# Optimization experiments

Hardware: AMD Instinct MI355X
Metric: run time of the kernel (lower is better)

Reference implementation:

```python
import jax, jax.numpy as jnp
import numpy as np

N_NODES = 100000
N_EDGES = 1600000
D_IN, D_HID, N_CLS, N_LAYERS = 128, 256, 10, 3


def setup_inputs() -> dict:
    key = jax.random.key(0)
    ks = jax.random.split(key, 8)
    x = jax.random.normal(ks[0], (N_NODES, D_IN), dtype=jnp.float32)
    edge_index = jax.random.randint(ks[1], (2, N_EDGES), 0, N_NODES, dtype=jnp.int64)
    s = 0.05
    Wl = jax.random.normal(ks[2], (N_LAYERS, D_HID, D_IN), dtype=jnp.float32) * s
    Wr = jax.random.normal(ks[3], (N_LAYERS, D_HID, D_IN), dtype=jnp.float32) * s
    bias = jnp.zeros((N_LAYERS, D_HID), dtype=jnp.float32)
    W1 = jax.random.normal(ks[4], (D_HID, D_HID), dtype=jnp.float32) * s
    b1 = jnp.zeros((D_HID,), dtype=jnp.float32)
    W2 = jax.random.normal(ks[5], (N_CLS, D_HID), dtype=jnp.float32) * s
    b2 = jnp.zeros((N_CLS,), dtype=jnp.float32)
    return {"x": x, "edge_index": edge_index, "Wl": Wl, "Wr": Wr, "bias": bias,
            "W1": W1, "b1": b1, "W2": W2, "b2": b2}


def reference(x, edge_index, Wl, Wr, bias, W1, b1, W2, b2):
    n = x.shape[0]
    src, tgt = edge_index[0], edge_index[1]
    # mean aggregation of source-node features onto targets (SAGEConv aggr='mean')
    deg = jax.ops.segment_sum(jnp.ones(src.shape[0], x.dtype), tgt, num_segments=n)
    agg = jax.ops.segment_sum(x[src], tgt, num_segments=n)  # [N, D_in]
    agg = agg / jnp.clip(deg, 1.0)[:, None]
    # Every layer consumes the ORIGINAL x (per the source forward), so agg is shared.
    h = None
    for l in range(Wl.shape[0]):
        h = jax.nn.relu(agg @ Wl[l].T + x @ Wr[l].T + bias[l])  # [N, D_hid]
    # global_mean_pool over all nodes (single graph)
    pooled = jnp.mean(h, axis=0, keepdims=True)  # [1, D_hid]
    z = jax.nn.relu(pooled @ W1.T + b1)
    z = z @ W2.T + b2
    return jax.nn.log_softmax(z, axis=1)
```

## Files before the change

### kernel.cpp

```cpp
#include <hip/hip_runtime.h>
#include <hip/hip_bf16.h>

#define D_IN  128
#define D_HID 256
#define CBITS 7
#define CSIZE 128
#define EPB   4096
#define CCAP  4096

typedef __bf16 bf16x8 __attribute__((ext_vector_type(8)));
typedef float  f32x4  __attribute__((ext_vector_type(4)));
typedef float  f32x2  __attribute__((ext_vector_type(2)));

__device__ __forceinline__ unsigned short f2bf(float f) {
    unsigned u = __float_as_uint(f);
    u += 0x7FFFu + ((u >> 16) & 1u);
    return (unsigned short)(u >> 16);
}
__device__ __forceinline__ uint2 pack4(float4 v) {
    unsigned lo = (unsigned)f2bf(v.x) | ((unsigned)f2bf(v.y) << 16);
    unsigned hi = (unsigned)f2bf(v.z) | ((unsigned)f2bf(v.w) << 16);
    return make_uint2(lo, hi);
}
__device__ __forceinline__ unsigned packfp8(float4 v) {
    int u = __builtin_amdgcn_cvt_pk_fp8_f32(v.x, v.y, 0, false);
    u = __builtin_amdgcn_cvt_pk_fp8_f32(v.z, v.w, u, true);
    return (unsigned)u;
}
__device__ __forceinline__ void g2lds16(const void* g, void* l) {
    __builtin_amdgcn_global_load_lds(
        (const __attribute__((address_space(1))) unsigned int*)g,
        (__attribute__((address_space(3))) unsigned int*)l, 16, 0, 0);
}
__device__ __forceinline__ void acc16(f32x2* a, uint4 v) {
    a[0] += __builtin_amdgcn_cvt_pk_f32_fp8(v.x, false);
    a[1] += __builtin_amdgcn_cvt_pk_f32_fp8(v.x, true);
    a[2] += __builtin_amdgcn_cvt_pk_f32_fp8(v.y, false);
    a[3] += __builtin_amdgcn_cvt_pk_f32_fp8(v.y, true);
    a[4] += __builtin_amdgcn_cvt_pk_f32_fp8(v.z, false);
    a[5] += __builtin_amdgcn_cvt_pk_f32_fp8(v.z, true);
    a[6] += __builtin_amdgcn_cvt_pk_f32_fp8(v.w, false);
    a[7] += __builtin_amdgcn_cvt_pk_f32_fp8(v.w, true);
}

__global__ __launch_bounds__(256)
void prep(const float* __restrict__ x, unsigned short* __restrict__ xb,
          unsigned char* __restrict__ x8,
          const float* __restrict__ Wr2, const float* __restrict__ Wl2,
          unsigned short* __restrict__ Bsw,
          int* __restrict__ gcur, float* __restrict__ pooled_pad,
          long n16, int NXB, int NCB) {
    const int bid = blockIdx.x;
    const int tid = threadIdx.x;
    if (bid < NXB) {
        const long t = (long)bid * 256 + tid;
        if (t >= n16) return;
        const float4* x4 = (const float4*)x;
        float4 v0 = x4[t * 4], v1 = x4[t * 4 + 1], v2 = x4[t * 4 + 2], v3 = x4[t * 4 + 3];
        uint2 p0 = pack4(v0), p1 = pack4(v1), p2 = pack4(v2), p3 = pack4(v3);
        ((uint4*)xb)[t * 2]     = make_uint4(p0.x, p0.y, p1.x, p1.y);
        ((uint4*)xb)[t * 2 + 1] = make_uint4(p2.x, p2.y, p3.x, p3.y);
        ((uint4*)x8)[t] = make_uint4(packfp8(v0), packfp8(v1), packfp8(v2), packfp8(v3));
    } else if (bid < NXB + 32) {
        const int t_idx = (bid - NXB) * 256 + tid;
        const int lane = t_idx & 63;
        const int rest = t_idx >> 6;
        const int tt   = rest & 3;
        const int wn2  = (rest >> 2) & 3;
        const int kk   = rest >> 4;
        const int j = wn2 * 64 + tt * 16 + (lane & 15);
        const int k = kk * 32 + (lane >> 4) * 8;
        const float* src = (k < 128) ? &Wr2[j * 128 + k] : &Wl2[j * 128 + (k - 128)];
        float4 v0 = *(const float4*)src;
        float4 v1 = *(const float4*)(src + 4);
        uint2 p0 = pack4(v0), p1 = pack4(v1);
        *(uint4*)&Bsw[(long)t_idx * 8] = make_uint4(p0.x, p0.y, p1.x, p1.y);
    } else {
        for (int i = tid; i < NCB * 16; i += 256) gcur[i] = 0;
        for (int i = tid; i < 256 * 16; i += 256) pooled_pad[i] = 0.f;
    }
}

__global__ __launch_bounds__(512)
void coarse_bin(const void* __restrict__ ei, int* __restrict__ gcur,
                unsigned* __restrict__ segc, int E, int NCB) {
    __shared__ unsigned sorted[EPB];
    __shared__ unsigned short bkt[EPB];
    __shared__ int cnt[1024], scn[1024], cur[1024], gbase[1024];
    __shared__ int s_is64;
    const int tid = threadIdx.x;
    const long e0 = (long)blockIdx.x * EPB;
    const int ecnt = (int)min((long)EPB, (long)E - e0);

    if (tid < 64) {
        const int v = ((const int*)ei)[2 * tid + 1];
        const unsigned long long b = __ballot(v != 0);
        if (tid == 0) s_is64 = (b == 0ull);
    }
    for (int i = tid; i < 1024; i += 512) cnt[i] = 0;
    __syncthreads();
    const int is64 = s_is64;

    int sv[8], tv[8];
    #pragma unroll
    for (int k = 0; k < 8; ++k) {
        const int j = tid + k * 512;
        if (j < ecnt) {
            if (is64) {
                sv[k] = (int)((const long long*)ei)[e0 + j];
                tv[k] = (int)((const long long*)ei)[E + e0 + j];
            } else {
                sv[k] = ((const int*)ei)[e0 + j];
                tv[k] = ((const int*)ei)[E + e0 + j];
            }
            atomicAdd(&cnt[tv[k] >> CBITS], 1);
        }
    }
    __syncthreads();

    scn[tid] = cnt[tid];
    scn[tid + 512] = cnt[tid + 512];
    __syncthreads();
    for (int off = 1; off < 1024; off <<= 1) {
        const int v0 = (tid >= off) ? scn[tid - off] : 0;
        const int v1 = (tid + 512 >= off) ? scn[tid + 512 - off] : 0;
        __syncthreads();
        scn[tid] += v0;
        scn[tid + 512] += v1;
        __syncthreads();
    }
    cur[tid] = scn[tid] - cnt[tid];
    cur[tid + 512] = scn[tid + 512] - cnt[tid + 512];
    for (int c = tid; c < NCB; c += 512)
        gbase[c] = cnt[c] ? atomicAdd(&gcur[c * 16], cnt[c]) : 0;
    __syncthreads();

    #pragma unroll
    for (int k = 0; k < 8; ++k) {
        const int j = tid + k * 512;
        if (j < ecnt) {
            const int c = tv[k] >> CBITS;
            const int r = atomicAdd(&cur[c], 1);
            sorted[r] = ((unsigned)sv[k] << CBITS) | (unsigned)(tv[k] & (CSIZE - 1));
            bkt[r] = (unsigned short)c;
        }
    }
    __syncthreads();

    for (int i = tid; i < ecnt; i += 512) {
        const int c = bkt[i];
        const int pos = gbase[c] + (i - (scn[c] - cnt[c]));
        if (pos < CCAP) segc[(long)c * CCAP + pos] = sorted[i];
    }
}

__global__ __launch_bounds__(512)
void refine_gather(const int* __restrict__ gcur, const unsigned* __restrict__ segc,
                   const unsigned char* __restrict__ x8,
                   unsigned short* __restrict__ aggb, int M) {
    __shared__ unsigned order[CCAP];
    __shared__ int degh[CSIZE], scn[CSIZE], cur[CSIZE];
    const int tid = threadIdx.x;
    const int cb = blockIdx.x;
    const int nbase = cb << CBITS;
    const int nn = min(CSIZE, M - nbase);
    const int len = min(gcur[cb * 16], CCAP);
    const unsigned* sp = segc + (long)cb * CCAP;

    if (tid < CSIZE) degh[tid] = 0;
    __syncthreads();
    for (int i = tid; i < len; i += 512) {
        const unsigned e = sp[i];
        atomicAdd(&degh[e & (CSIZE - 1)], 1);
    }
    __syncthreads();
    if (tid < CSIZE) scn[tid] = degh[tid];
    __syncthreads();
    for (int off = 1; off < CSIZE; off <<= 1) {
        int v = 0;
        if (tid >= off && tid < CSIZE) v = scn[tid - off];
        __syncthreads();
        if (tid < CSIZE) scn[tid] += v;
        __syncthreads();
    }
    if (tid < CSIZE) cur[tid] = scn[tid] - degh[tid];
    __syncthreads();
    for (int i = tid; i < len; i += 512) {
        const unsigned e = sp[i];
        const int r = atomicAdd(&cur[e & (CSIZE - 1)], 1);
        order[r] = e & ~(unsigned)(CSIZE - 1);
    }
    __syncthreads();

    const int lane = tid & 63;
    const int wave = tid >> 6;
    const int ns   = lane >> 3;
    const int c4   = lane & 7;
    const unsigned chb = (unsigned)c4 * 16;

    for (int base = wave * 8; base < nn; base += 64) {
        const int nl = base + ns;
        int deg = 0, beg = 0;
        if (nl < nn) { deg = degh[nl]; beg = scn[nl] - deg; }
        f32x2 a[8] = {}, b[8] = {};
        int i = 0;
        for (; i + 4 <= deg; i += 4) {
            const unsigned o0 = order[beg + i];
            const unsigned o1 = order[beg + i + 1];
            const unsigned o2 = order[beg + i + 2];
            const unsigned o3 = order[beg + i + 3];
            uint4 v0 = *(const uint4*)(x8 + (o0 + chb));
            uint4 v1 = *(const uint4*)(x8 + (o1 + chb));
            uint4 v2 = *(const uint4*)(x8 + (o2 + chb));
            uint4 v3 = *(const uint4*)(x8 + (o3 + chb));
            acc16(a, v0); acc16(b, v1); acc16(a, v2); acc16(b, v3);
        }
        if (i < deg) {
            uint4 v = *(const uint4*)(x8 + (order[beg + i] + chb));
            acc16(a, v); ++i;
        }
        if (i < deg) {
            uint4 v = *(const uint4*)(x8 + (order[beg + i] + chb));
            acc16(b, v); ++i;
        }
        if (i < deg) {
            uint4 v = *(const uint4*)(x8 + (order[beg + i] + chb));
            acc16(a, v); ++i;
        }
        if (nl < nn) {
            const float rdiv = 1.0f / fmaxf((float)deg, 1.0f);
            unsigned w[8];
            #pragma unroll
            for (int j = 0; j < 8; ++j) {
                const f32x2 s = a[j] + b[j];
                w[j] = (unsigned)f2bf(s.x * rdiv) | ((unsigned)f2bf(s.y * rdiv) << 16);
            }
            unsigned short* dst = aggb + (long)(nbase + nl) * 128 + c4 * 16;
            *(uint4*)dst       = make_uint4(w[0], w[1], w[2], w[3]);
            *(uint4*)(dst + 8) = make_uint4(w[4], w[5], w[6], w[7]);
        }
    }
}

__global__ __launch_bounds__(256, 2)
void gemm_pool(const unsigned short* __restrict__ xb, const unsigned short* __restrict__ aggb,
               const unsigned short* __restrict__ Bsw, const float* __restrict__ bias2,
               float* __restrict__ pooled_pad, int M, int NT) {
    __shared__ unsigned short As[4 * 32 * 256];
    const int tid  = threadIdx.x;
    const int lane = tid & 63;
    const int wn2  = tid >> 6;
    const int lrow = lane & 15;
    const int quad = lane >> 4;
    const int bid  = blockIdx.x;
    const int GRID = gridDim.x;
    const int nt   = (NT - bid + GRID - 1) / GRID;
    if (nt <= 0) return;

    uint4 bb[8][4];
    #pragma unroll
    for (int kk = 0; kk < 8; ++kk)
        #pragma unroll
        for (int t = 0; t < 4; ++t)
            bb[kk][t] = *(const uint4*)&Bsw[((((long)kk * 4 + wn2) * 4 + t) * 64 + lane) * 8];
    float bv[4];
    #pragma unroll
    for (int t = 0; t < 4; ++t) bv[t] = bias2[wn2 * 64 + t * 16 + lrow];

    const int cl = tid & 31;
    const int rw = tid >> 5;
    const int cs = cl ^ rw;
    const unsigned short* sbase = (cs < 16) ? (xb + (long)cs * 8)
                                            : (aggb + (long)(cs - 16) * 8);
    char* lbase = (char*)As + rw * 512 + cl * 16;

    auto STAGE = [&](int p) {
        const long trow = ((long)bid + (long)p * GRID) * 32;
        char* ld = lbase + (p & 3) * 16384;
        #pragma unroll
        for (int s = 0; s < 4; ++s)
            g2lds16(sbase + (trow + s * 8 + rw) * 128, ld + s * 4096);
    };

    #pragma unroll
    for (int p = 0; p < 3; ++p) if (p < nt) STAGE(p);

    float ps[4] = {0.f, 0.f, 0.f, 0.f};

    for (int p = 0; p < nt; ++p) {
        const int rem = nt - 1 - p;
        if (rem >= 2)      asm volatile("s_waitcnt vmcnt(8)" ::: "memory");
        else if (rem == 1) asm volatile("s_waitcnt vmcnt(4)" ::: "memory");
        else               asm volatile("s_waitcnt vmcnt(0)" ::: "memory");
        __builtin_amdgcn_s_barrier();
        if (p + 3 < nt) STAGE(p + 3);

        const char* Ab = (const char*)As + (p & 3) * 16384;
        f32x4 acc[2][4] = {};
        #pragma unroll
        for (int kk = 0; kk < 8; ++kk) {
            uint4 aC[2];
            #pragma unroll
            for (int i = 0; i < 2; ++i) {
                const int r = i * 16 + lrow;
                aC[i] = *(const uint4*)(Ab + r * 512 + (((kk * 4 + quad) ^ (lrow & 7)) * 16));
            }
            #pragma unroll
            for (int i = 0; i < 2; ++i)
                #pragma unroll
                for (int t = 0; t < 4; ++t)
                    acc[i][t] = __builtin_amdgcn_mfma_f32_16x16x32_bf16(
                        *(bf16x8*)&aC[i], *(bf16x8*)&bb[kk][t], acc[i][t], 0, 0, 0);
        }

        const long trow = ((long)bid + (long)p * GRID) * 32;
        #pragma unroll
        for (int t = 0; t < 4; ++t) {
            float s = 0.f;
            #pragma unroll
            for (int i = 0; i < 2; ++i) {
                const long rbase = trow + i * 16 + quad * 4;
                #pragma unroll
                for (int r = 0; r < 4; ++r) {
                    float h = fmaxf(acc[i][t][r] + bv[t], 0.f);
                    if (rbase + r < M) s += h;
                }
            }
            ps[t] += s;
        }
    }

    #pragma unroll
    for (int t = 0; t < 4; ++t) {
        ps[t] += __shfl_xor(ps[t], 16);
        ps[t] += __shfl_xor(ps[t], 32);
        if (quad == 0)
            atomicAdd(&pooled_pad[(wn2 * 64 + t * 16 + lrow) * 16], ps[t]);
    }
}

__global__ __launch_bounds__(256)
void head_kernel(const float* __restrict__ pooled_pad,
                 const float* __restrict__ W1, const float* __restrict__ b1,
                 const float* __restrict__ W2, const float* __restrict__ b2,
                 float* __restrict__ out, float invM) {
    __shared__ float pooled_s[256];
    __shared__ float z1_s[256];
    __shared__ float z2_s[10];
    const int j = threadIdx.x;

    pooled_s[j] = pooled_pad[j * 16] * invM;
    __syncthreads();

    const float4* w4 = (const float4*)(W1 + (long)j * 256);
    float sx = 0.f, sy = 0.f, sz = 0.f, sw = 0.f;
    #pragma unroll 8
    for (int k = 0; k < 64; ++k) {
        float4 w = w4[k];
        float4 p = *(const float4*)&pooled_s[k * 4];
        sx += w.x * p.x; sy += w.y * p.y; sz += w.z * p.z; sw += w.w * p.w;
    }
    z1_s[j] = fmaxf(b1[j] + sx + sy + sz + sw, 0.f);
    __syncthreads();

    if (j < 160) {
        const int c = j >> 4, q = j & 15;
        float s = 0.f;
        for (int k = q; k < 256; k += 16) s += W2[c * 256 + k] * z1_s[k];
        #pragma unroll
        for (int off = 8; off >= 1; off >>= 1) s += __shfl_down(s, off, 16);
        if (q == 0) z2_s[c] = s + b2[c];
    }
    __syncthreads();

    if (j == 0) {
        float mx = z2_s[0];
        for (int c = 1; c < 10; ++c) mx = fmaxf(mx, z2_s[c]);
        float se = 0.f;
        for (int c = 0; c < 10; ++c) se += expf(z2_s[c] - mx);
        const float ls = logf(se);
        for (int c = 0; c < 10; ++c) out[c] = z2_s[c] - mx - ls;
    }
}

extern "C" void kernel_launch(void* const* d_in, const int* in_sizes, int n_in,
                              void* d_out, int out_size, void* d_ws, size_t ws_size,
                              hipStream_t stream) {
    const float* x    = (const float*)d_in[0];
    const void*  ei   = d_in[1];
    const float* Wl   = (const float*)d_in[2];
    const float* Wr   = (const float*)d_in[3];
    const float* bias = (const float*)d_in[4];
    const float* W1   = (const float*)d_in[5];
    const float* b1   = (const float*)d_in[6];
    const float* W2   = (const float*)d_in[7];
    const float* b2   = (const float*)d_in[8];
    float* out = (float*)d_out;

    const int M = in_sizes[0] / D_IN;
    const int E = in_sizes[1] / 2;
    const int L = in_sizes[4] / D_HID;
    const int NMB = (M + 127) / 128;
    const long Mpad = (long)NMB * 128;
    const int NCB = (M + CSIZE - 1) / CSIZE;
    const int NB1 = (E + EPB - 1) / EPB;
    const int NT  = (M + 31) / 32;
    const int NG  = (NT < 512) ? NT : 512;

    const float* Wl2   = Wl + (long)(L - 1) * D_HID * D_IN;
    const float* Wr2   = Wr + (long)(L - 1) * D_HID * D_IN;
    const float* bias2 = bias + (long)(L - 1) * D_HID;

    unsigned short* xb   = (unsigned short*)d_ws;
    unsigned short* aggb = xb + Mpad * D_IN;
    unsigned char*  x8   = (unsigned char*)(aggb + Mpad * D_IN);
    unsigned short* Bsw  = (unsigned short*)(x8 + Mpad * D_IN);
    float* pooled_pad    = (float*)(Bsw + 256 * 256);
    int*      gcur       = (int*)(pooled_pad + 256 * 16);
    unsigned* segc       = (unsigned*)(gcur + (long)NCB * 16);

    const long n16 = (long)M * 8;
    const int NXB = (int)((n16 + 255) / 256);

    prep<<<NXB + 32 + 1, 256, 0, stream>>>(x, xb, x8, Wr2, Wl2, Bsw, gcur, pooled_pad,
                                           n16, NXB, NCB);
    coarse_bin<<<NB1, 512, 0, stream>>>(ei, gcur, segc, E, NCB);
    refine_gather<<<NCB, 512, 0, stream>>>(gcur, segc, x8, aggb, M);

    gemm_pool<<<NG, 256, 0, stream>>>(xb, aggb, Bsw, bias2, pooled_pad, M, NT);

    head_kernel<<<1, 256, 0, stream>>>(pooled_pad, W1, b1, W2, b2, out, 1.0f / (float)M);
}
```

Baseline: 214.8 us.

## Fuse prep with coarse binning and fold head into gemm via last-block counter

Merges the conversion/prep kernel and the coarse edge-binning kernel into one launch, with zeroing moved to a memset. The MLP head now runs inside gemm_pool, in the last block to finish, detected by an atomic done counter. This cuts two kernel launches and their inter-kernel gaps. In exchange it adds a memset, a threadfence and an atomic per block, and the prep blocks now reserve the binning kernel's large shared memory, which may lower their occupancy.

```diff
diff --git a/kernel.cpp b/kernel.cpp
--- a/kernel.cpp
+++ b/kernel.cpp
@@ -43,17 +43,23 @@
     a[7] += __builtin_amdgcn_cvt_pk_f32_fp8(v.w, true);
 }
 
-__global__ __launch_bounds__(256)
-void prep(const float* __restrict__ x, unsigned short* __restrict__ xb,
-          unsigned char* __restrict__ x8,
-          const float* __restrict__ Wr2, const float* __restrict__ Wl2,
-          unsigned short* __restrict__ Bsw,
-          int* __restrict__ gcur, float* __restrict__ pooled_pad,
-          long n16, int NXB, int NCB) {
+__global__ __launch_bounds__(512)
+void prep_bin(const float* __restrict__ x, unsigned short* __restrict__ xb,
+              unsigned char* __restrict__ x8,
+              const float* __restrict__ Wr2, const float* __restrict__ Wl2,
+              unsigned short* __restrict__ Bsw,
+              const void* __restrict__ ei, int* __restrict__ gcur,
+              unsigned* __restrict__ segc,
+              long n16, int NXB2, int E, int NCB) {
+    __shared__ unsigned sorted[EPB];
+    __shared__ unsigned short bkt[EPB];
+    __shared__ int cnt[1024], scn[1024], cur[1024], gbase[1024];
+    __shared__ int s_is64;
     const int bid = blockIdx.x;
     const int tid = threadIdx.x;
-    if (bid < NXB) {
-        const long t = (long)bid * 256 + tid;
+
+    if (bid < NXB2) {
+        const long t = (long)bid * 512 + tid;
         if (t >= n16) return;
         const float4* x4 = (const float4*)x;
         float4 v0 = x4[t * 4], v1 = x4[t * 4 + 1], v2 = x4[t * 4 + 2], v3 = x4[t * 4 + 3];
@@ -61,8 +67,10 @@
         ((uint4*)xb)[t * 2]     = make_uint4(p0.x, p0.y, p1.x, p1.y);
         ((uint4*)xb)[t * 2 + 1] = make_uint4(p2.x, p2.y, p3.x, p3.y);
         ((uint4*)x8)[t] = make_uint4(packfp8(v0), packfp8(v1), packfp8(v2), packfp8(v3));
-    } else if (bid < NXB + 32) {
-        const int t_idx = (bid - NXB) * 256 + tid;
+        return;
+    }
+    if (bid < NXB2 + 16) {
+        const int t_idx = (bid - NXB2) * 512 + tid;
         const int lane = t_idx & 63;
         const int rest = t_idx >> 6;
         const int tt   = rest & 3;
@@ -75,21 +83,11 @@
         float4 v1 = *(const float4*)(src + 4);
         uint2 p0 = pack4(v0), p1 = pack4(v1);
         *(uint4*)&Bsw[(long)t_idx * 8] = make_uint4(p0.x, p0.y, p1.x, p1.y);
-    } else {
-        for (int i = tid; i < NCB * 16; i += 256) gcur[i] = 0;
-        for (int i = tid; i < 256 * 16; i += 256) pooled_pad[i] = 0.f;
-    }
-}
-
-__global__ __launch_bounds__(512)
-void coarse_bin(const void* __restrict__ ei, int* __restrict__ gcur,
-                unsigned* __restrict__ segc, int E, int NCB) {
-    __shared__ unsigned sorted[EPB];
-    __shared__ unsigned short bkt[EPB];
-    __shared__ int cnt[1024], scn[1024], cur[1024], gbase[1024];
-    __shared__ int s_is64;
-    const int tid = threadIdx.x;
-    const long e0 = (long)blockIdx.x * EPB;
+        return;
+    }
+
+    const int cbid = bid - NXB2 - 16;
+    const long e0 = (long)cbid * EPB;
     const int ecnt = (int)min((long)EPB, (long)E - e0);
 
     if (tid < 64) {
@@ -245,7 +243,10 @@
 __global__ __launch_bounds__(256, 2)
 void gemm_pool(const unsigned short* __restrict__ xb, const unsigned short* __restrict__ aggb,
                const unsigned short* __restrict__ Bsw, const float* __restrict__ bias2,
-               float* __restrict__ pooled_pad, int M, int NT) {
+               float* __restrict__ pooled_pad, int* __restrict__ done,
+               const float* __restrict__ W1, const float* __restrict__ b1,
+               const float* __restrict__ W2, const float* __restrict__ b2,
+               float* __restrict__ out, float invM, int M, int NT) {
     __shared__ unsigned short As[4 * 32 * 256];
     const int tid  = threadIdx.x;
     const int lane = tid & 63;
@@ -255,101 +256,103 @@
     const int bid  = blockIdx.x;
     const int GRID = gridDim.x;
     const int nt   = (NT - bid + GRID - 1) / GRID;
-    if (nt <= 0) return;
-
-    uint4 bb[8][4];
-    #pragma unroll
-    for (int kk = 0; kk < 8; ++kk)
+
+    if (nt > 0) {
+        uint4 bb[8][4];
         #pragma unroll
-        for (int t = 0; t < 4; ++t)
-            bb[kk][t] = *(const uint4*)&Bsw[((((long)kk * 4 + wn2) * 4 + t) * 64 + lane) * 8];
-    float bv[4];
-    #pragma unroll
-    for (int t = 0; t < 4; ++t) bv[t] = bias2[wn2 * 64 + t * 16 + lrow];
-
-    const int cl = tid & 31;
-    const int rw = tid >> 5;
-    const int cs = cl ^ rw;
-    const unsigned short* sbase = (cs < 16) ? (xb + (long)cs * 8)
-                                            : (aggb + (long)(cs - 16) * 8);
-    char* lbase = (char*)As + rw * 512 + cl * 16;
-
-    auto STAGE = [&](int p) {
-        const long trow = ((long)bid + (long)p * GRID) * 32;
-        char* ld = lbase + (p & 3) * 16384;
+        for (int kk = 0; kk < 8; ++kk)
+            #pragma unroll
+            for (int t = 0; t < 4; ++t)
+                bb[kk][t] = *(const uint4*)&Bsw[((((long)kk * 4 + wn2) * 4 + t) * 64 + lane) * 8];
+        float bv[4];
         #pragma unroll
-        for (int s = 0; s < 4; ++s)
-            g2lds16(sbase + (trow + s * 8 + rw) * 128, ld + s * 4096);
-    };
-
-    #pragma unroll
-    for (int p = 0; p < 3; ++p) if (p < nt) STAGE(p);
-
-    float ps[4] = {0.f, 0.f, 0.f, 0.f};
-
-    for (int p = 0; p < nt; ++p) {
-        const int rem = nt - 1 - p;
-        if (rem >= 2)      asm volatile("s_waitcnt vmcnt(8)" ::: "memory");
-        else if (rem == 1) asm volatile("s_waitcnt vmcnt(4)" ::: "memory");
-        else               asm volatile("s_waitcnt vmcnt(0)" ::: "memory");
-        __builtin_amdgcn_s_barrier();
-        if (p + 3 < nt) STAGE(p + 3);
-
-        const char* Ab = (const char*)As + (p & 3) * 16384;
-        f32x4 acc[2][4] = {};
+        for (int t = 0; t < 4; ++t) bv[t] = bias2[wn2 * 64 + t * 16 + lrow];
+
+        const int cl = tid & 31;
+        const int rw = tid >> 5;
+        const int cs = cl ^ rw;
+        const unsigned short* sbase = (cs < 16) ? (xb + (long)cs * 8)
+                                                : (aggb + (long)(cs - 16) * 8);
+        char* lbase = (char*)As + rw * 512 + cl * 16;
+
+        auto STAGE = [&](int p) {
+            const long trow = ((long)bid + (long)p * GRID) * 32;
+            char* ld = lbase + (p & 3) * 16384;
+            #pragma unroll
+            for (int s = 0; s < 4; ++s)
+                g2lds16(sbase + (trow + s * 8 + rw) * 128, ld + s * 4096);
+        };
+
         #pragma unroll
-        for (int kk = 0; kk < 8; ++kk) {
-            uint4 aC[2];
+        for (int p = 0; p < 3; ++p) if (p < nt) STAGE(p);
+
+        float ps[4] = {0.f, 0.f, 0.f, 0.f};
+
+        for (int p = 0; p < nt; ++p) {
+            const int rem = nt - 1 - p;
+            if (rem >= 2)      asm volatile("s_waitcnt vmcnt(8)" ::: "memory");
+            else if (rem == 1) asm volatile("s_waitcnt vmcnt(4)" ::: "memory");
+            else               asm volatile("s_waitcnt vmcnt(0)" ::: "memory");
+            __builtin_amdgcn_s_barrier();
+            if (p + 3 < nt) STAGE(p + 3);
+
+            const char* Ab = (const char*)As + (p & 3) * 16384;
+            f32x4 acc[2][4] = {};
             #pragma unroll
-            for (int i = 0; i < 2; ++i) {
-                const int r = i * 16 + lrow;
-                aC[i] = *(const uint4*)(Ab + r * 512 + (((kk * 4 + quad) ^ (lrow & 7)) * 16));
+            for (int kk = 0; kk < 8; ++kk) {
+                uint4 aC[2];
+                #pragma unroll
+                for (int i = 0; i < 2; ++i) {
+                    const int r = i * 16 + lrow;
+                    aC[i] = *(const uint4*)(Ab + r * 512 + (((kk * 4 + quad) ^ (lrow & 7)) * 16));
+                }
+                #pragma unroll
+                for (int i = 0; i < 2; ++i)
+                    #pragma unroll
+                    for (int t = 0; t < 4; ++t)
+                        acc[i][t] = __builtin_amdgcn_mfma_f32_16x16x32_bf16(
+                            *(bf16x8*)&aC[i], *(bf16x8*)&bb[kk][t], acc[i][t], 0, 0, 0);
             }
+
+            const long trow = ((long)bid + (long)p * GRID) * 32;
             #pragma unroll
-            for (int i = 0; i < 2; ++i)
+            for (int t = 0; t < 4; ++t) {
+                float s = 0.f;
                 #pragma unroll
-                for (int t = 0; t < 4; ++t)
-                    acc[i][t] = __builtin_amdgcn_mfma_f32_16x16x32_bf16(
-                        *(bf16x8*)&aC[i], *(bf16x8*)&bb[kk][t], acc[i][t], 0, 0, 0);
-        }
-
-        const long trow = ((long)bid + (long)p * GRID) * 32;
+                for (int i = 0; i < 2; ++i) {
+                    const long rbase = trow + i * 16 + quad * 4;
+                    #pragma unroll
+                    for (int r = 0; r < 4; ++r) {
+                        float h = fmaxf(acc[i][t][r] + bv[t], 0.f);
+                        if (rbase + r < M) s += h;
+                    }
+                }
+                ps[t] += s;
+            }
+        }
+
         #pragma unroll
         for (int t = 0; t < 4; ++t) {
-            float s = 0.f;
-            #pragma unroll
-            for (int i = 0; i < 2; ++i) {
-                const long rbase = trow + i * 16 + quad * 4;
-                #pragma unroll
-                for (int r = 0; r < 4; ++r) {
-                    float h = fmaxf(acc[i][t][r] + bv[t], 0.f);
-                    if (rbase + r < M) s += h;
-                }
-            }
-            ps[t] += s;
-        }
-    }
-
-    #pragma unroll
-    for (int t = 0; t < 4; ++t) {
-        ps[t] += __shfl_xor(ps[t], 16);
-        ps[t] += __shfl_xor(ps[t], 32);
-        if (quad == 0)
-            atomicAdd(&pooled_pad[(wn2 * 64 + t * 16 + lrow) * 16], ps[t]);
-    }
-}
-
-__global__ __launch_bounds__(256)
-void head_kernel(const float* __restrict__ pooled_pad,
-                 const float* __restrict__ W1, const float* __restrict__ b1,
-                 const float* __restrict__ W2, const float* __restrict__ b2,
-                 float* __restrict__ out, float invM) {
+            ps[t] += __shfl_xor(ps[t], 16);
+            ps[t] += __shfl_xor(ps[t], 32);
+            if (quad == 0)
+                atomicAdd(&pooled_pad[(wn2 * 64 + t * 16 + lrow) * 16], ps[t]);
+        }
+    }
+
+    __threadfence();
+    __shared__ int s_last;
+    if (tid == 0) s_last = (atomicAdd(done, 1) == (int)gridDim.x - 1);
+    __syncthreads();
+    if (!s_last) return;
+    __threadfence();
+
     __shared__ float pooled_s[256];
     __shared__ float z1_s[256];
     __shared__ float z2_s[10];
-    const int j = threadIdx.x;
-
-    pooled_s[j] = pooled_pad[j * 16] * invM;
+    const int j = tid;
+
+    pooled_s[j] = atomicAdd(&pooled_pad[j * 16], 0.0f) * invM;
     __syncthreads();
 
     const float4* w4 = (const float4*)(W1 + (long)j * 256);
@@ -417,17 +420,18 @@
     unsigned short* Bsw  = (unsigned short*)(x8 + Mpad * D_IN);
     float* pooled_pad    = (float*)(Bsw + 256 * 256);
     int*      gcur       = (int*)(pooled_pad + 256 * 16);
-    unsigned* segc       = (unsigned*)(gcur + (long)NCB * 16);
+    int*      done       = gcur + (long)NCB * 16;
+    unsigned* segc       = (unsigned*)(done + 16);
 
     const long n16 = (long)M * 8;
-    const int NXB = (int)((n16 + 255) / 256);
-
-    prep<<<NXB + 32 + 1, 256, 0, stream>>>(x, xb, x8, Wr2, Wl2, Bsw, gcur, pooled_pad,
-                                           n16, NXB, NCB);
-    coarse_bin<<<NB1, 512, 0, stream>>>(ei, gcur, segc, E, NCB);
+    const int NXB2 = (int)((n16 + 511) / 512);
+
+    hipMemsetAsync(pooled_pad, 0, 256 * 16 * 4 + (size_t)NCB * 16 * 4 + 16 * 4, stream);
+
+    prep_bin<<<NXB2 + 16 + NB1, 512, 0, stream>>>(x, xb, x8, Wr2, Wl2, Bsw,
+                                                  ei, gcur, segc, n16, NXB2, E, NCB);
     refine_gather<<<NCB, 512, 0, stream>>>(gcur, segc, x8, aggb, M);
 
-    gemm_pool<<<NG, 256, 0, stream>>>(xb, aggb, Bsw, bias2, pooled_pad, M, NT);
-
-    head_kernel<<<1, 256, 0, stream>>>(pooled_pad, W1, b1, W2, b2, out, 1.0f / (float)M);
-}
+    gemm_pool<<<NG, 256, 0, stream>>>(xb, aggb, Bsw, bias2, pooled_pad, done,
+                                      W1, b1, W2, b2, out, 1.0f / (float)M, M, NT);
+}
```

New measurement: 230.6 us. 7.3% more time.
